# Optimization experiments

Hardware: AMD Instinct MI355X
Metric: run time of the kernel (lower is better)

Reference implementation:

```python
import jax, jax.numpy as jnp
import numpy as np

T, B, D = 32, 16, 128


def _evolve(xr, xi, U):
    # xr, xi: [T,B,D,D]; U: [D,D,2] -> complex U x U^H per matrix
    Ur, Ui = U[..., 0], U[..., 1]
    r = jnp.einsum('ij,tbjk->tbik', Ur, xr) - jnp.einsum('ij,tbjk->tbik', Ui, xi)
    i = jnp.einsum('ij,tbjk->tbik', Ui, xr) + jnp.einsum('ij,tbjk->tbik', Ur, xi)
    out_r = jnp.einsum('tbik,jk->tbij', r, Ur) + jnp.einsum('tbik,jk->tbij', i, Ui)
    out_i = jnp.einsum('tbik,jk->tbij', i, Ur) - jnp.einsum('tbik,jk->tbij', r, Ui)
    return out_r, out_i


def _forward(inputs_real, inputs_imag, Uq, Uk, Uv):
    qr, qi = _evolve(inputs_real, inputs_imag, Uq)
    kr, ki = _evolve(inputs_real, inputs_imag, Uk)
    vr, vi = _evolve(inputs_real, inputs_imag, Uv)
    # trace(A @ B) = sum_ij A_ij * B_ji -> distance scores [Tq, Tk, B]
    tr_r = jnp.einsum('qbij,kbji->qkb', qr, kr) - jnp.einsum('qbij,kbji->qkb', qi, ki)
    tr_i = jnp.einsum('qbij,kbji->qkb', qr, ki) + jnp.einsum('qbij,kbji->qkb', qi, kr)
    dist = jnp.sqrt(tr_r * tr_r + tr_i * tr_i)
    # original builds scores via torch.tensor(list) -> values are detached
    dist = jax.lax.stop_gradient(dist)
    # original applies softmax over the LAST dim of the [Tk, B] score matrix,
    # i.e. over the batch dim (faithful reproduction)
    S = jax.nn.softmax(dist, axis=-1)  # [Tq, Tk, B]
    # original zip(values[0], values[1], scores) iterates the (real, imag)
    # components of the value at t=0 and t=1 against score rows 0 and 1
    s0 = S[:, 0, :, None, None]  # [Tq,B,1,1]
    s1 = S[:, 1, :, None, None]
    out_r = vr[0][None] * s0 + vi[0][None] * s1  # [Tq,B,D,D]
    out_i = vr[1][None] * s0 + vi[1][None] * s1
    return out_r, out_i


def setup_inputs() -> dict:
    key = jax.random.key(0)
    k0, k1, k2, k3, k4 = jax.random.split(key, 5)
    inputs_real = jax.random.normal(k0, (T, B, D, D), dtype=jnp.float32)
    inputs_imag = jax.random.normal(k1, (T, B, D, D), dtype=jnp.float32)
    eye = jnp.stack([jnp.eye(D, dtype=jnp.float32), jnp.zeros((D, D), jnp.float32)], axis=-1)
    Uq = eye + 0.05 * jax.random.normal(k2, (D, D, 2), dtype=jnp.float32)
    Uk = eye + 0.05 * jax.random.normal(k3, (D, D, 2), dtype=jnp.float32)
    Uv = eye + 0.05 * jax.random.normal(k4, (D, D, 2), dtype=jnp.float32)
    return {"inputs_real": inputs_real, "inputs_imag": inputs_imag, "Uq": Uq, "Uk": Uk, "Uv": Uv}


def reference(inputs_real, inputs_imag, Uq, Uk, Uv):
    return _forward(inputs_real, inputs_imag, Uq, Uk, Uv)
```

## Files before the change

### kernel.cpp

```cpp
#include <hip/hip_runtime.h>
#include <math.h>

#define TT 32
#define BB 16
#define DD 128
#define MAT 16384
#define OFF_MR   0
#define OFF_MI   16384
#define OFF_YTR  32768
#define OFF_YTI  (32768 + 64*16384)
#define OFF_ZSR  (OFF_YTI + 64*16384)
#define OFF_ZSI  (OFF_ZSR + 32*16384)
#define OFF_VR   (OFF_ZSI + 32*16384)
#define OFF_VI   (OFF_VR + 32*16384)
#define OFF_TR   (OFF_VI + 32*16384)
#define OFF_S    (OFF_TR + 2048)

__device__ __forceinline__ float dot4(float4 a, float4 b) {
    return a.x*b.x + a.y*b.y + a.z*b.z + a.w*b.w;
}

__global__ __launch_bounds__(128) void k_M(const float* __restrict__ Uq,
                                           const float* __restrict__ Uk,
                                           float* __restrict__ ws) {
    const int i = blockIdx.x;
    const int j = threadIdx.x;
    __shared__ float qr_s[128], qi_s[128];
    qr_s[j] = Uq[(j*128 + i)*2 + 0];
    qi_s[j] = Uq[(j*128 + i)*2 + 1];
    __syncthreads();
    const float2* Uk2 = (const float2*)Uk;
    float mr = 0.f, mi = 0.f;
    #pragma unroll 8
    for (int p = 0; p < 128; ++p) {
        float2 k2 = Uk2[p*128 + j];
        float qr = qr_s[p], qi = qi_s[p];
        mr += qr*k2.x + qi*k2.y;
        mi += qr*k2.y - qi*k2.x;
    }
    ws[OFF_MR + i*128 + j] = mr;
    ws[OFF_MI + i*128 + j] = mi;
}

#define AT_PAD 36
template<int STAGE>
__global__ __launch_bounds__(256) void k_evolve(const float* __restrict__ xr,
                                                const float* __restrict__ xi,
                                                const float* __restrict__ Uv,
                                                float* __restrict__ ws) {
    const int bid = blockIdx.x;
    const int m   = bid >> 2;
    const int i0  = (bid & 3) * 32;
    const int tid = threadIdx.x;
    const int rg  = tid >> 5;
    const int cg  = tid & 31;

    __shared__ __align__(16) float smem_f[2304*2 + 4096*2];
    float* At_r = smem_f;
    float* At_i = smem_f + 2304;
    float* Bbuf = smem_f + 4608;
    float* T_r = smem_f;
    float* T_i = smem_f + 32*129;

    float accr[4][4], acci[4][4];
    #pragma unroll
    for (int r = 0; r < 4; ++r)
        #pragma unroll
        for (int k = 0; k < 4; ++k) { accr[r][k] = 0.f; acci[r][k] = 0.f; }

    const float* Br;
    const float* Bi;
    if (STAGE == 0) { Br = xr + (m & 31) * MAT;      Bi = xi + (m & 31) * MAT; }
    else            { Br = ws + OFF_YTR + m * MAT;   Bi = ws + OFF_YTI + m * MAT; }
    const float4* Br4 = (const float4*)Br;
    const float4* Bi4 = (const float4*)Bi;

    auto loadA = [&](int h) {
        #pragma unroll
        for (int w = 0; w < 8; ++w) {
            int idx = w*256 + tid;
            int r = idx >> 6;
            int p = idx & 63;
            float ar, ai;
            if (m < 32) {
                ar = ws[OFF_MR + (i0+r)*128 + h*64 + p];
                ai = ws[OFF_MI + (i0+r)*128 + h*64 + p];
            } else {
                float2 u = ((const float2*)Uv)[(i0+r)*128 + h*64 + p];
                ar = u.x; ai = u.y;
            }
            At_r[p*AT_PAD + r] = ar;
            At_i[p*AT_PAD + r] = ai;
        }
    };

    float4 pr0, pr1, pi0, pi1;
    auto gloadB = [&](int t) {
        int b0 = t*512;
        pr0 = Br4[b0 + tid];
        pr1 = Br4[b0 + 256 + tid];
        pi0 = Bi4[b0 + tid];
        pi1 = Bi4[b0 + 256 + tid];
    };
    auto writeB = [&](int buf) {
        float4* dR = (float4*)(Bbuf + buf*4096);
        float4* dI = (float4*)(Bbuf + buf*4096 + 2048);
        dR[tid]       = pr0;
        dR[tid + 256] = pr1;
        dI[tid]       = pi0;
        dI[tid + 256] = pi1;
    };

    loadA(0);
    gloadB(0);
    writeB(0);

    for (int t = 0; t < 8; ++t) {
        if (t < 7) gloadB(t+1);
        __syncthreads();
        if (t == 4) { loadA(1); __syncthreads(); }
        const float* bufR = Bbuf + (t&1)*4096;
        const float* bufI = bufR + 2048;
        #pragma unroll
        for (int pp = 0; pp < 16; ++pp) {
            const int pl = ((t & 3) << 4) + pp;
            const float4 ar4 = *(const float4*)&At_r[pl*AT_PAD + (rg<<2)];
            const float4 ai4 = *(const float4*)&At_i[pl*AT_PAD + (rg<<2)];
            const float4 brv = *(const float4*)&bufR[pp*128 + (cg<<2)];
            const float4 biv = *(const float4*)&bufI[pp*128 + (cg<<2)];
#define CROW(R, AR, AI)                                                          \
    do {                                                                         \
        const float aR_ = (AR), aI_ = (AI);                                      \
        const float br_[4] = {brv.x, brv.y, brv.z, brv.w};                       \
        const float bi_[4] = {biv.x, biv.y, biv.z, biv.w};                       \
        _Pragma("unroll")                                                        \
        for (int k = 0; k < 4; ++k) {                                            \
            if (STAGE == 0) { accr[R][k] += aR_*br_[k] - aI_*bi_[k];             \
                              acci[R][k] += aR_*bi_[k] + aI_*br_[k]; }           \
            else            { accr[R][k] += aR_*br_[k] + aI_*bi_[k];             \
                              acci[R][k] += aR_*bi_[k] - aI_*br_[k]; }           \
        }                                                                        \
    } while (0)
            CROW(0, ar4.x, ai4.x);
            CROW(1, ar4.y, ai4.y);
            CROW(2, ar4.z, ai4.z);
            CROW(3, ar4.w, ai4.w);
#undef CROW
        }
        if (t < 7) writeB((t+1)&1);
    }

    const bool transpose_store = (STAGE == 0) || (m >= 32);
    if (transpose_store) {
        __syncthreads();
        #pragma unroll
        for (int r = 0; r < 4; ++r)
            #pragma unroll
            for (int k = 0; k < 4; ++k) {
                T_r[((rg<<2)+r)*129 + (cg<<2)+k] = accr[r][k];
                T_i[((rg<<2)+r)*129 + (cg<<2)+k] = acci[r][k];
            }
        __syncthreads();
        float* dstR; float* dstI;
        if (STAGE == 0) { dstR = ws + OFF_YTR + m*MAT;      dstI = ws + OFF_YTI + m*MAT; }
        else            { dstR = ws + OFF_VR + (m-32)*MAT;  dstI = ws + OFF_VI + (m-32)*MAT; }
        #pragma unroll
        for (int w = 0; w < 16; ++w) {
            int o = w*256 + tid;
            int c = o >> 5, ii = o & 31;
            dstR[c*128 + i0 + ii] = T_r[ii*129 + c];
            dstI[c*128 + i0 + ii] = T_i[ii*129 + c];
        }
    } else {
        float* dstR = ws + OFF_ZSR + m*MAT;
        float* dstI = ws + OFF_ZSI + m*MAT;
        #pragma unroll
        for (int r = 0; r < 4; ++r) {
            float4 vR = make_float4(accr[r][0], accr[r][1], accr[r][2], accr[r][3]);
            float4 vI = make_float4(acci[r][0], acci[r][1], acci[r][2], acci[r][3]);
            *(float4*)&dstR[(i0 + (rg<<2) + r)*128 + (cg<<2)] = vR;
            *(float4*)&dstI[(i0 + (rg<<2) + r)*128 + (cg<<2)] = vI;
        }
    }
}

__global__ __launch_bounds__(256) void k_trace(const float* __restrict__ xr,
                                               const float* __restrict__ xi,
                                               float* __restrict__ ws) {
    const int q = blockIdx.x >> 4, b = blockIdx.x & 15;
    const int tid = threadIdx.x;
    const float4* Xr4  = (const float4*)(xr + (q*16 + b)*MAT);
    const float4* Xi4  = (const float4*)(xi + (q*16 + b)*MAT);
    const float4* Z0r4 = (const float4*)(ws + OFF_ZSR + b*MAT);
    const float4* Z0i4 = (const float4*)(ws + OFF_ZSI + b*MAT);
    const float4* Z1r4 = (const float4*)(ws + OFF_ZSR + (16+b)*MAT);
    const float4* Z1i4 = (const float4*)(ws + OFF_ZSI + (16+b)*MAT);
    float r0 = 0.f, s0 = 0.f, r1 = 0.f, s1 = 0.f;
    #pragma unroll 4
    for (int w = 0; w < 16; ++w) {
        int e = w*256 + tid;
        float4 xrv = Xr4[e], xiv = Xi4[e];
        float4 z0r = Z0r4[e], z0i = Z0i4[e];
        float4 z1r = Z1r4[e], z1i = Z1i4[e];
        r0 += dot4(xrv, z0r) - dot4(xiv, z0i);
        s0 += dot4(xrv, z0i) + dot4(xiv, z0r);
        r1 += dot4(xrv, z1r) - dot4(xiv, z1i);
        s1 += dot4(xrv, z1i) + dot4(xiv, z1r);
    }
    #pragma unroll
    for (int off = 32; off > 0; off >>= 1) {
        r0 += __shfl_down(r0, off);
        s0 += __shfl_down(s0, off);
        r1 += __shfl_down(r1, off);
        s1 += __shfl_down(s1, off);
    }
    __shared__ float red[4][4];
    if ((tid & 63) == 0) {
        int wv = tid >> 6;
        red[wv][0] = r0; red[wv][1] = s0; red[wv][2] = r1; red[wv][3] = s1;
    }
    __syncthreads();
    if (tid == 0) {
        float a0 = red[0][0]+red[1][0]+red[2][0]+red[3][0];
        float a1 = red[0][1]+red[1][1]+red[2][1]+red[3][1];
        float a2 = red[0][2]+red[1][2]+red[2][2]+red[3][2];
        float a3 = red[0][3]+red[1][3]+red[2][3]+red[3][3];
        float* trp = ws + OFF_TR;
        trp[((q*2+0)*16 + b)*2 + 0] = a0;
        trp[((q*2+0)*16 + b)*2 + 1] = a1;
        trp[((q*2+1)*16 + b)*2 + 0] = a2;
        trp[((q*2+1)*16 + b)*2 + 1] = a3;
    }
}

__global__ __launch_bounds__(64) void k_softmax(float* __restrict__ ws) {
    const int t = threadIdx.x;
    const float* trp = ws + OFF_TR + t*32;
    float d[16];
    float mx = -1e30f;
    #pragma unroll
    for (int b = 0; b < 16; ++b) {
        float rr = trp[b*2+0], ii = trp[b*2+1];
        d[b] = sqrtf(rr*rr + ii*ii);
        mx = fmaxf(mx, d[b]);
    }
    float sum = 0.f;
    #pragma unroll
    for (int b = 0; b < 16; ++b) { d[b] = expf(d[b] - mx); sum += d[b]; }
    float inv = 1.f / sum;
    #pragma unroll
    for (int b = 0; b < 16; ++b) ws[OFF_S + t*16 + b] = d[b] * inv;
}

__global__ __launch_bounds__(256) void k_out(const float* __restrict__ ws,
                                             float* __restrict__ out) {
    const int t = blockIdx.x >> 4, b = blockIdx.x & 15;
    const float s0 = ws[OFF_S + (t*2+0)*16 + b];
    const float s1 = ws[OFF_S + (t*2+1)*16 + b];
    const float4* Vr0 = (const float4*)(ws + OFF_VR + b*MAT);
    const float4* Vi0 = (const float4*)(ws + OFF_VI + b*MAT);
    const float4* Vr1 = (const float4*)(ws + OFF_VR + (16+b)*MAT);
    const float4* Vi1 = (const float4*)(ws + OFF_VI + (16+b)*MAT);
    float4* outR = (float4*)out + (t*16 + b)*4096;
    float4* outI = (float4*)out + 2097152 + (t*16 + b)*4096;
    #pragma unroll 4
    for (int w = 0; w < 16; ++w) {
        int e = w*256 + threadIdx.x;
        float4 a = Vr0[e], bb = Vi0[e], c = Vr1[e], dd = Vi1[e];
        outR[e] = make_float4(a.x*s0 + bb.x*s1, a.y*s0 + bb.y*s1,
                              a.z*s0 + bb.z*s1, a.w*s0 + bb.w*s1);
        outI[e] = make_float4(c.x*s0 + dd.x*s1, c.y*s0 + dd.y*s1,
                              c.z*s0 + dd.z*s1, c.w*s0 + dd.w*s1);
    }
}

extern "C" void kernel_launch(void* const* d_in, const int* in_sizes, int n_in,
                              void* d_out, int out_size, void* d_ws, size_t ws_size,
                              hipStream_t stream) {
    const float* xr = (const float*)d_in[0];
    const float* xi = (const float*)d_in[1];
    const float* Uq = (const float*)d_in[2];
    const float* Uk = (const float*)d_in[3];
    const float* Uv = (const float*)d_in[4];
    float* ws  = (float*)d_ws;
    float* out = (float*)d_out;

    k_M<<<128, 128, 0, stream>>>(Uq, Uk, ws);
    k_evolve<0><<<256, 256, 0, stream>>>(xr, xi, Uv, ws);
    k_evolve<1><<<256, 256, 0, stream>>>(xr, xi, Uv, ws);
    k_trace<<<512, 256, 0, stream>>>(xr, xi, ws);
    k_softmax<<<1, 64, 0, stream>>>(ws);
    k_out<<<512, 256, 0, stream>>>(ws, out);
}
```

Baseline: 92.32 us.

## Halve evolve row tile to 16 rows and interleave complex A in shared memory

The evolve kernels now give each block 16 output rows instead of 32 and launch 512 blocks instead of 256, so more CUs have work. Each thread holds a 2x4 complex tile instead of 4x4. The A operand is stored once for all 128 k values as interleaved real/imag pairs, loaded with one float4, which removes the mid-loop reload and its extra barrier. The cost is that each block re-reads the full B matrix for half as many output rows, doubling global traffic for B, and each shared-memory B load feeds fewer FMAs.

```diff
diff --git a/kernel.cpp b/kernel.cpp
--- a/kernel.cpp
+++ b/kernel.cpp
@@ -42,29 +42,27 @@
     ws[OFF_MI + i*128 + j] = mi;
 }
 
-#define AT_PAD 36
 template<int STAGE>
 __global__ __launch_bounds__(256) void k_evolve(const float* __restrict__ xr,
                                                 const float* __restrict__ xi,
                                                 const float* __restrict__ Uv,
                                                 float* __restrict__ ws) {
     const int bid = blockIdx.x;
-    const int m   = bid >> 2;
-    const int i0  = (bid & 3) * 32;
+    const int m   = bid >> 3;
+    const int i0  = (bid & 7) * 16;
     const int tid = threadIdx.x;
-    const int rg  = tid >> 5;
-    const int cg  = tid & 31;
-
-    __shared__ __align__(16) float smem_f[2304*2 + 4096*2];
-    float* At_r = smem_f;
-    float* At_i = smem_f + 2304;
-    float* Bbuf = smem_f + 4608;
+    const int rg  = tid & 7;
+    const int cg  = tid >> 3;
+
+    __shared__ __align__(16) float smem_f[4096 + 8192];
+    float* At   = smem_f;
+    float* Bbuf = smem_f + 4096;
     float* T_r = smem_f;
-    float* T_i = smem_f + 32*129;
-
-    float accr[4][4], acci[4][4];
-    #pragma unroll
-    for (int r = 0; r < 4; ++r)
+    float* T_i = smem_f + 16*132;
+
+    float accr[2][4], acci[2][4];
+    #pragma unroll
+    for (int r = 0; r < 2; ++r)
         #pragma unroll
         for (int k = 0; k < 4; ++k) { accr[r][k] = 0.f; acci[r][k] = 0.f; }
 
@@ -75,24 +73,26 @@
     const float4* Br4 = (const float4*)Br;
     const float4* Bi4 = (const float4*)Bi;
 
-    auto loadA = [&](int h) {
-        #pragma unroll
-        for (int w = 0; w < 8; ++w) {
-            int idx = w*256 + tid;
-            int r = idx >> 6;
-            int p = idx & 63;
-            float ar, ai;
+    {
+        #pragma unroll
+        for (int w = 0; w < 4; ++w) {
+            int slot = w*256 + tid;
+            int r8 = slot & 7;
+            int p  = slot >> 3;
+            float ar0, ai0, ar1, ai1;
             if (m < 32) {
-                ar = ws[OFF_MR + (i0+r)*128 + h*64 + p];
-                ai = ws[OFF_MI + (i0+r)*128 + h*64 + p];
+                ar0 = ws[OFF_MR + (i0 + r8*2    )*128 + p];
+                ai0 = ws[OFF_MI + (i0 + r8*2    )*128 + p];
+                ar1 = ws[OFF_MR + (i0 + r8*2 + 1)*128 + p];
+                ai1 = ws[OFF_MI + (i0 + r8*2 + 1)*128 + p];
             } else {
-                float2 u = ((const float2*)Uv)[(i0+r)*128 + h*64 + p];
-                ar = u.x; ai = u.y;
+                float2 u0 = ((const float2*)Uv)[(i0 + r8*2    )*128 + p];
+                float2 u1 = ((const float2*)Uv)[(i0 + r8*2 + 1)*128 + p];
+                ar0 = u0.x; ai0 = u0.y; ar1 = u1.x; ai1 = u1.y;
             }
-            At_r[p*AT_PAD + r] = ar;
-            At_i[p*AT_PAD + r] = ai;
-        }
-    };
+            *(float4*)&At[p*32 + r8*4] = make_float4(ar0, ai0, ar1, ai1);
+        }
+    }
 
     float4 pr0, pr1, pi0, pi1;
     auto gloadB = [&](int t) {
@@ -111,41 +111,36 @@
         dI[tid + 256] = pi1;
     };
 
-    loadA(0);
     gloadB(0);
     writeB(0);
 
     for (int t = 0; t < 8; ++t) {
         if (t < 7) gloadB(t+1);
         __syncthreads();
-        if (t == 4) { loadA(1); __syncthreads(); }
         const float* bufR = Bbuf + (t&1)*4096;
         const float* bufI = bufR + 2048;
         #pragma unroll
         for (int pp = 0; pp < 16; ++pp) {
-            const int pl = ((t & 3) << 4) + pp;
-            const float4 ar4 = *(const float4*)&At_r[pl*AT_PAD + (rg<<2)];
-            const float4 ai4 = *(const float4*)&At_i[pl*AT_PAD + (rg<<2)];
+            const int p = (t<<4) + pp;
+            const float4 a4  = *(const float4*)&At[p*32 + (rg<<2)];
             const float4 brv = *(const float4*)&bufR[pp*128 + (cg<<2)];
             const float4 biv = *(const float4*)&bufI[pp*128 + (cg<<2)];
-#define CROW(R, AR, AI)                                                          \
-    do {                                                                         \
-        const float aR_ = (AR), aI_ = (AI);                                      \
-        const float br_[4] = {brv.x, brv.y, brv.z, brv.w};                       \
-        const float bi_[4] = {biv.x, biv.y, biv.z, biv.w};                       \
-        _Pragma("unroll")                                                        \
-        for (int k = 0; k < 4; ++k) {                                            \
-            if (STAGE == 0) { accr[R][k] += aR_*br_[k] - aI_*bi_[k];             \
-                              acci[R][k] += aR_*bi_[k] + aI_*br_[k]; }           \
-            else            { accr[R][k] += aR_*br_[k] + aI_*bi_[k];             \
-                              acci[R][k] += aR_*bi_[k] - aI_*br_[k]; }           \
-        }                                                                        \
-    } while (0)
-            CROW(0, ar4.x, ai4.x);
-            CROW(1, ar4.y, ai4.y);
-            CROW(2, ar4.z, ai4.z);
-            CROW(3, ar4.w, ai4.w);
-#undef CROW
+            const float br_[4] = {brv.x, brv.y, brv.z, brv.w};
+            const float bi_[4] = {biv.x, biv.y, biv.z, biv.w};
+            #pragma unroll
+            for (int k = 0; k < 4; ++k) {
+                if (STAGE == 0) {
+                    accr[0][k] += a4.x*br_[k] - a4.y*bi_[k];
+                    acci[0][k] += a4.x*bi_[k] + a4.y*br_[k];
+                    accr[1][k] += a4.z*br_[k] - a4.w*bi_[k];
+                    acci[1][k] += a4.z*bi_[k] + a4.w*br_[k];
+                } else {
+                    accr[0][k] += a4.x*br_[k] + a4.y*bi_[k];
+                    acci[0][k] += a4.x*bi_[k] - a4.y*br_[k];
+                    accr[1][k] += a4.z*br_[k] + a4.w*bi_[k];
+                    acci[1][k] += a4.z*bi_[k] - a4.w*br_[k];
+                }
+            }
         }
         if (t < 7) writeB((t+1)&1);
     }
@@ -154,32 +149,33 @@
     if (transpose_store) {
         __syncthreads();
         #pragma unroll
-        for (int r = 0; r < 4; ++r)
+        for (int r = 0; r < 2; ++r)
             #pragma unroll
             for (int k = 0; k < 4; ++k) {
-                T_r[((rg<<2)+r)*129 + (cg<<2)+k] = accr[r][k];
-                T_i[((rg<<2)+r)*129 + (cg<<2)+k] = acci[r][k];
+                T_r[(rg*2 + r)*132 + cg*4 + k] = accr[r][k];
+                T_i[(rg*2 + r)*132 + cg*4 + k] = acci[r][k];
             }
         __syncthreads();
         float* dstR; float* dstI;
         if (STAGE == 0) { dstR = ws + OFF_YTR + m*MAT;      dstI = ws + OFF_YTI + m*MAT; }
         else            { dstR = ws + OFF_VR + (m-32)*MAT;  dstI = ws + OFF_VI + (m-32)*MAT; }
         #pragma unroll
-        for (int w = 0; w < 16; ++w) {
+        for (int w = 0; w < 8; ++w) {
             int o = w*256 + tid;
-            int c = o >> 5, ii = o & 31;
-            dstR[c*128 + i0 + ii] = T_r[ii*129 + c];
-            dstI[c*128 + i0 + ii] = T_i[ii*129 + c];
+            int c  = o >> 4;
+            int ii = o & 15;
+            dstR[c*128 + i0 + ii] = T_r[ii*132 + c];
+            dstI[c*128 + i0 + ii] = T_i[ii*132 + c];
         }
     } else {
         float* dstR = ws + OFF_ZSR + m*MAT;
         float* dstI = ws + OFF_ZSI + m*MAT;
         #pragma unroll
-        for (int r = 0; r < 4; ++r) {
+        for (int r = 0; r < 2; ++r) {
             float4 vR = make_float4(accr[r][0], accr[r][1], accr[r][2], accr[r][3]);
             float4 vI = make_float4(acci[r][0], acci[r][1], acci[r][2], acci[r][3]);
-            *(float4*)&dstR[(i0 + (rg<<2) + r)*128 + (cg<<2)] = vR;
-            *(float4*)&dstI[(i0 + (rg<<2) + r)*128 + (cg<<2)] = vI;
+            *(float4*)&dstR[(i0 + rg*2 + r)*128 + cg*4] = vR;
+            *(float4*)&dstI[(i0 + rg*2 + r)*128 + cg*4] = vI;
         }
     }
 }
@@ -286,8 +282,8 @@
     float* out = (float*)d_out;
 
     k_M<<<128, 128, 0, stream>>>(Uq, Uk, ws);
-    k_evolve<0><<<256, 256, 0, stream>>>(xr, xi, Uv, ws);
-    k_evolve<1><<<256, 256, 0, stream>>>(xr, xi, Uv, ws);
+    k_evolve<0><<<512, 256, 0, stream>>>(xr, xi, Uv, ws);
+    k_evolve<1><<<512, 256, 0, stream>>>(xr, xi, Uv, ws);
     k_trace<<<512, 256, 0, stream>>>(xr, xi, ws);
     k_softmax<<<1, 64, 0, stream>>>(ws);
     k_out<<<512, 256, 0, stream>>>(ws, out);
```

After: 93.84 us. No clear change (+1.6%).
